# Kernel optimization log

Measured on AMD Instinct MI355X. Metric: run time of the kernel, lower is better.

Reference implementation:

```python
import jax, jax.numpy as jnp
import numpy as np
from jax import lax

B, C, K = 16, 320, 8  # batch, channels, template kernel size
EPS = 1e-12  # F.normalize eps


def _pool_to(x, k):
    # adaptive avg pool to (k, k); H, W are exact multiples of k here
    b, c, h, w = x.shape
    return x.reshape(b, c, k, h // k, k, w // k).mean(axis=(3, 5))


def _l2norm(x):
    # L2 normalize over channel dim (dim=1), matching F.normalize(p=2, dim=1)
    n = jnp.sqrt(jnp.sum(x * x, axis=1, keepdims=True))
    return x / jnp.maximum(n, EPS)


def _fusion(feats, w1, b1, w2, b2):
    # global avg pool -> 2-layer MLP score per template -> softmax -> weighted sum
    scores = jnp.concatenate(
        [jax.nn.relu(f.mean(axis=(2, 3)) @ w1 + b1) @ w2 + b2 for f in feats], axis=1
    )  # (B, 3)
    a = jax.nn.softmax(scores, axis=1)
    return sum(a[:, i, None, None, None] * feats[i] for i in range(3))


def _corr(template_kernel, search):
    # depthwise correlation + channel sum == per-sample VALID conv with a
    # single (1, C, K, K) kernel; vmap over batch
    tn = _l2norm(template_kernel)  # (B, C, K, K)
    sn = _l2norm(search)           # (B, C, H, W)

    def one(sb, tb):
        return lax.conv_general_dilated(
            sb[None], tb[None], (1, 1), 'VALID',
            dimension_numbers=('NCHW', 'OIHW', 'NCHW'))[0]  # (1, Ho, Wo)

    return jax.vmap(one)(sn, tn)  # (B, 1, Ho, Wo)


_SPECS = [
    ('t0_p3', (B, C, 32, 32)), ('t0_p4', (B, C, 16, 16)), ('t0_p5', (B, C, 8, 8)),
    ('t1_p3', (B, C, 32, 32)), ('t1_p4', (B, C, 16, 16)), ('t1_p5', (B, C, 8, 8)),
    ('t2_p3', (B, C, 32, 32)), ('t2_p4', (B, C, 16, 16)), ('t2_p5', (B, C, 8, 8)),
    ('s_p3', (B, C, 64, 64)), ('s_p4', (B, C, 32, 32)), ('s_p5', (B, C, 16, 16)),
]
_PARAMS = [
    ('fp3_w1', (C, C // 4)), ('fp3_b1', (C // 4,)), ('fp3_w2', (C // 4, 1)), ('fp3_b2', (1,)),
    ('fp4_w1', (C, C // 4)), ('fp4_b1', (C // 4,)), ('fp4_w2', (C // 4, 1)), ('fp4_b2', (1,)),
    ('fp5_w1', (C, C // 4)), ('fp5_b1', (C // 4,)), ('fp5_w2', (C // 4, 1)), ('fp5_b2', (1,)),
]


def setup_inputs() -> dict:
    key = jax.random.key(0)
    d = {}
    for i, (name, shape) in enumerate(_SPECS):
        d[name] = jax.random.normal(jax.random.fold_in(key, i), shape, jnp.float32)
    for j, (name, shape) in enumerate(_PARAMS):
        k = jax.random.fold_in(key, 100 + j)
        if name.endswith('b1') or name.endswith('b2'):
            d[name] = jnp.zeros(shape, jnp.float32)
        else:
            d[name] = jax.random.normal(k, shape, jnp.float32) * 0.05
    return d


def reference(t0_p3, t0_p4, t0_p5, t1_p3, t1_p4, t1_p5, t2_p3, t2_p4, t2_p5,
              s_p3, s_p4, s_p5,
              fp3_w1, fp3_b1, fp3_w2, fp3_b2,
              fp4_w1, fp4_b1, fp4_w2, fp4_b2,
              fp5_w1, fp5_b1, fp5_w2, fp5_b2):
    tp3 = _fusion([t0_p3, t1_p3, t2_p3], fp3_w1, fp3_b1, fp3_w2, fp3_b2)
    tp4 = _fusion([t0_p4, t1_p4, t2_p4], fp4_w1, fp4_b1, fp4_w2, fp4_b2)
    tp5 = _fusion([t0_p5, t1_p5, t2_p5], fp5_w1, fp5_b1, fp5_w2, fp5_b2)
    corr_p3 = _corr(_pool_to(tp3, K), s_p3)  # (B, 1, 57, 57)
    corr_p4 = _corr(_pool_to(tp4, K), s_p4)  # (B, 1, 25, 25)
    corr_p5 = _corr(_pool_to(tp5, K), s_p5)  # (B, 1, 9, 9)
    return (corr_p3, corr_p4, corr_p5)
```

## Files before the change

### kernel.cpp

```cpp
#include <hip/hip_runtime.h>
#include <math.h>

#define BATCH 16
#define CH 320

typedef __attribute__((ext_vector_type(8))) short bf16x8;
typedef __attribute__((ext_vector_type(4))) short shortx4;
typedef __attribute__((ext_vector_type(4))) float f32x4;

static constexpr size_t PLSZ     = (size_t)BATCH * CH * 64;
static constexpr size_t WS_POOL3 = 0;
static constexpr size_t WS_POOL4 = 3 * PLSZ;
static constexpr size_t WS_TF    = 6 * PLSZ;
static constexpr size_t WS_MEANS = 9 * PLSZ;
static constexpr size_t WS_AW    = WS_MEANS + 9 * BATCH * CH;
static constexpr size_t WS_PART  = WS_AW + 144;
static constexpr size_t WS_ABF   = WS_PART + 3 * BATCH * 80 * 64;
static constexpr size_t UB3 = 0;
static constexpr size_t UB4 = (size_t)BATCH * 64 * 4096;
static constexpr size_t UB5 = UB4 + (size_t)BATCH * 64 * 1024;

__device__ __forceinline__ float bf2f(unsigned short u) {
    union { unsigned int i; float f; } x; x.i = ((unsigned int)u) << 16; return x.f;
}
__device__ __forceinline__ unsigned short f2bf(float f) {
    union { float f; unsigned int i; } x; x.f = f;
    return (unsigned short)((x.i + 0x7FFFu + ((x.i >> 16) & 1u)) >> 16);
}

template <int HW, int KK>
__device__ __forceinline__ void pool_body(int idx, const float* __restrict__ a0,
                                          const float* __restrict__ a1, const float* __restrict__ a2,
                                          float* __restrict__ dst, float* __restrict__ means, int lane) {
    constexpr int NPL = BATCH * CH * 64;
    int tmpl = idx / NPL;
    int r = idx % NPL;
    const float* src = (tmpl == 0) ? a0 : ((tmpl == 1) ? a1 : a2);
    int bc = r >> 6;
    int pos = r & 63;
    int oh = pos >> 3, ow = pos & 7;
    const float* base = src + (size_t)bc * HW * HW;
    float s = 0.0f;
    if constexpr (KK == 4) {
#pragma unroll
        for (int i = 0; i < 4; ++i) {
            float4 v = *(const float4*)(base + (oh * 4 + i) * HW + ow * 4);
            s += v.x + v.y + v.z + v.w;
        }
    } else {
#pragma unroll
        for (int i = 0; i < 2; ++i) {
            float2 v = *(const float2*)(base + (oh * 2 + i) * HW + ow * 2);
            s += v.x + v.y;
        }
    }
    s *= (1.0f / (KK * KK));
    dst[idx] = s;
    float m = s;
#pragma unroll
    for (int o = 32; o; o >>= 1) m += __shfl_xor(m, o);
    if (lane == 0) means[tmpl * (BATCH * CH) + bc] = m * (1.0f / 64.0f);
}

__global__ __launch_bounds__(256) void prep_kernel(
    const float* __restrict__ t0p3, const float* __restrict__ t1p3, const float* __restrict__ t2p3,
    const float* __restrict__ t0p4, const float* __restrict__ t1p4, const float* __restrict__ t2p4,
    const float* __restrict__ t0p5, const float* __restrict__ t1p5, const float* __restrict__ t2p5,
    float* __restrict__ pool3, float* __restrict__ pool4, float* __restrict__ means) {
    int bid = blockIdx.x, t = threadIdx.x, lane = t & 63;
    if (bid < 3840) {
        pool_body<32, 4>(bid * 256 + t, t0p3, t1p3, t2p3, pool3, means, lane);
    } else if (bid < 7680) {
        pool_body<16, 2>((bid - 3840) * 256 + t, t0p4, t1p4, t2p4, pool4, means + 3 * BATCH * CH, lane);
    } else {
        int w = ((bid - 7680) * 256 + t) >> 6;
        constexpr int NR = BATCH * CH;
        int tmpl = w / NR, rem = w % NR;
        const float* src = (tmpl == 0) ? t0p5 : ((tmpl == 1) ? t1p5 : t2p5);
        float v = src[(size_t)rem * 64 + lane];
#pragma unroll
        for (int o = 32; o; o >>= 1) v += __shfl_xor(v, o);
        if (lane == 0) means[6 * BATCH * CH + w] = v * (1.0f / 64.0f);
    }
}

__global__ __launch_bounds__(256) void weights_kernel(const float* __restrict__ means,
        const float* w13, const float* b13, const float* w23, const float* b23,
        const float* w14, const float* b14, const float* w24, const float* b24,
        const float* w15, const float* b15, const float* w25, const float* b25,
        float* __restrict__ a_out) {
    __shared__ float m[3 * CH];
    __shared__ float hv[240];
    __shared__ float sc[3];
    int lvl = blockIdx.x / BATCH;
    int b = blockIdx.x % BATCH;
    int t = threadIdx.x;
    const float* w1 = (lvl == 0) ? w13 : ((lvl == 1) ? w14 : w15);
    const float* b1 = (lvl == 0) ? b13 : ((lvl == 1) ? b14 : b15);
    const float* w2 = (lvl == 0) ? w23 : ((lvl == 1) ? w24 : w25);
    const float* b2 = (lvl == 0) ? b23 : ((lvl == 1) ? b24 : b25);
    const float* mb = means + lvl * (3 * BATCH * CH);
    for (int j = t; j < 3 * CH; j += 256) {
        int i = j / CH, c = j % CH;
        m[j] = mb[i * (BATCH * CH) + b * CH + c];
    }
    __syncthreads();
    if (t < 240) {
        int i = t / 80, jj = t % 80;
        float acc = b1[jj];
#pragma unroll 4
        for (int c = 0; c < CH; ++c) acc = fmaf(m[i * CH + c], w1[c * 80 + jj], acc);
        hv[t] = fmaxf(acc, 0.0f) * w2[jj];
    }
    __syncthreads();
    if (t < 3) {
        float s = b2[0];
#pragma unroll 8
        for (int jj = 0; jj < 80; ++jj) s += hv[t * 80 + jj];
        sc[t] = s;
    }
    __syncthreads();
    if (t == 0) {
        float mx = fmaxf(sc[0], fmaxf(sc[1], sc[2]));
        float e0 = expf(sc[0] - mx), e1 = expf(sc[1] - mx), e2 = expf(sc[2] - mx);
        float inv = 1.0f / (e0 + e1 + e2);
        float* ao = a_out + lvl * 48 + b * 3;
        ao[0] = e0 * inv; ao[1] = e1 * inv; ao[2] = e2 * inv;
    }
}

__global__ __launch_bounds__(256) void fuse_kernel(
        const float* __restrict__ p30, const float* __restrict__ p31, const float* __restrict__ p32,
        const float* __restrict__ p40, const float* __restrict__ p41, const float* __restrict__ p42,
        const float* __restrict__ p50, const float* __restrict__ p51, const float* __restrict__ p52,
        const float* __restrict__ aw, float* __restrict__ tf, float* __restrict__ partial) {
    __shared__ float red[256];
    int lvl = blockIdx.x / 1280;
    int r = blockIdx.x % 1280;
    int t = threadIdx.x;
    const float* p0 = (lvl == 0) ? p30 : ((lvl == 1) ? p40 : p50);
    const float* p1 = (lvl == 0) ? p31 : ((lvl == 1) ? p41 : p51);
    const float* p2 = (lvl == 0) ? p32 : ((lvl == 1) ? p42 : p52);
    int idx = r * 256 + t;
    int b = r / 80;
    int j = r % 80;
    const float* ab = aw + lvl * 48 + b * 3;
    float a0 = ab[0], a1 = ab[1], a2 = ab[2];
    float v = a0 * p0[idx] + a1 * p1[idx] + a2 * p2[idx];
    tf[(size_t)lvl * PLSZ + idx] = v;
    red[t] = v * v;
    __syncthreads();
    if (t < 64) {
        float s = red[t] + red[t + 64] + red[t + 128] + red[t + 192];
        partial[((size_t)(lvl * BATCH + b) * 80 + j) * 64 + t] = s;
    }
}

__global__ __launch_bounds__(256) void atrans_kernel(const float* __restrict__ tf,
        const float* __restrict__ part, short* __restrict__ abf) {
    __shared__ float lds[64 * 68];
    __shared__ float red2[4 * 64];
    __shared__ float sv[64];
    int lvl = blockIdx.x >> 4;
    int b = blockIdx.x & 15;
    int t = threadIdx.x;
    {
        const float* p = part + ((size_t)(lvl * BATCH + b) * 80) * 64 + (t & 63);
        int jg = t >> 6;
        float s = 0.0f;
        for (int j = jg * 20; j < jg * 20 + 20; ++j) s += p[j * 64];
        red2[jg * 64 + (t & 63)] = s;
    }
    __syncthreads();
    if (t < 64) {
        float s = red2[t] + red2[64 + t] + red2[128 + t] + red2[192 + t];
        sv[t] = 1.0f / fmaxf(sqrtf(s), 1e-12f);
    }
    __syncthreads();
    const float* tb = tf + (size_t)lvl * PLSZ + (size_t)b * (CH * 64);
    short* ab = abf + ((size_t)(lvl * BATCH + b) * 64) * 320;
    for (int c0 = 0; c0 < 320; c0 += 64) {
        __syncthreads();
#pragma unroll
        for (int i = 0; i < 4; ++i) {
            int c = (t >> 4) + 16 * i;
            int p4 = (t & 15) * 4;
            *(float4*)(lds + c * 68 + p4) = *(const float4*)(tb + (size_t)(c0 + c) * 64 + p4);
        }
        __syncthreads();
        int p = t >> 2;
        int cs = (t & 3) * 16;
        float s_p = sv[p];
        bf16x8 o0, o1;
#pragma unroll
        for (int u = 0; u < 8; ++u) o0[u] = (short)f2bf(lds[(cs + u) * 68 + p] * s_p);
#pragma unroll
        for (int u = 0; u < 8; ++u) o1[u] = (short)f2bf(lds[(cs + 8 + u) * 68 + p] * s_p);
        *(bf16x8*)(ab + (size_t)p * 320 + c0 + cs) = o0;
        *(bf16x8*)(ab + (size_t)p * 320 + c0 + cs + 8) = o1;
    }
}

template <int H>
__device__ __forceinline__ void gemm_body(const float* __restrict__ S, const short* __restrict__ A,
                                          short* __restrict__ U, int bid,
                                          short* __restrict__ Bb, float* __restrict__ red,
                                          float* __restrict__ invs) {
    constexpr int N = H * H;
    constexpr int NBLK = N / 64;
    int b = bid / NBLK;
    int n0 = (bid % NBLK) * 64;
    int t = threadIdx.x;
    int w = t >> 6, l = t & 63, g = l >> 4, ln = l & 15;
    int cg = t >> 4;
    int nc = t & 15;
    const float* Sb = S + (size_t)b * CH * N + n0;
    const short* Ab = A + (size_t)b * 64 * 320;
    f32x4 acc[4];
#pragma unroll
    for (int i = 0; i < 4; ++i) acc[i] = (f32x4){0.f, 0.f, 0.f, 0.f};
    float ssq[4] = {0.f, 0.f, 0.f, 0.f};

    for (int kk = 0; kk < 320; kk += 32) {
        __syncthreads();
#pragma unroll
        for (int i = 0; i < 2; ++i) {
            int c = cg + 16 * i;
            float4 v = *(const float4*)(Sb + (size_t)(kk + c) * N + nc * 4);
            ssq[0] = fmaf(v.x, v.x, ssq[0]);
            ssq[1] = fmaf(v.y, v.y, ssq[1]);
            ssq[2] = fmaf(v.z, v.z, ssq[2]);
            ssq[3] = fmaf(v.w, v.w, ssq[3]);
            shortx4 h;
            h.x = (short)f2bf(v.x); h.y = (short)f2bf(v.y);
            h.z = (short)f2bf(v.z); h.w = (short)f2bf(v.w);
            *(shortx4*)(Bb + c * 76 + nc * 4) = h;
        }
        __syncthreads();
        bf16x8 af[4];
#pragma unroll
        for (int mt = 0; mt < 4; ++mt)
            af[mt] = *(const bf16x8*)(Ab + (mt * 16 + ln) * 320 + kk + 8 * g);
        bf16x8 bfr;
#pragma unroll
        for (int j = 0; j < 8; ++j) bfr[j] = Bb[(8 * g + j) * 76 + 16 * w + ln];
#pragma unroll
        for (int mt = 0; mt < 4; ++mt)
            acc[mt] = __builtin_amdgcn_mfma_f32_16x16x32_bf16(af[mt], bfr, acc[mt], 0, 0, 0);
    }
    red[cg * 64 + nc * 4 + 0] = ssq[0];
    red[cg * 64 + nc * 4 + 1] = ssq[1];
    red[cg * 64 + nc * 4 + 2] = ssq[2];
    red[cg * 64 + nc * 4 + 3] = ssq[3];
    __syncthreads();
    if (t < 64) {
        float s = 0.0f;
#pragma unroll
        for (int i = 0; i < 16; ++i) s += red[i * 64 + t];
        invs[t] = 1.0f / fmaxf(sqrtf(s), 1e-12f);
    }
    __syncthreads();
    float iv = invs[16 * w + ln];
#pragma unroll
    for (int mt = 0; mt < 4; ++mt) {
#pragma unroll
        for (int r = 0; r < 4; ++r) {
            int p = mt * 16 + 4 * g + r;
            U[(size_t)(b * 64 + p) * N + n0 + 16 * w + ln] = (short)f2bf(acc[mt][r] * iv);
        }
    }
}

__global__ __launch_bounds__(256) void gemm_kernel(const float* __restrict__ sp3,
        const float* __restrict__ sp4, const float* __restrict__ sp5,
        const short* __restrict__ abf, short* __restrict__ u) {
    __shared__ short Bb[32 * 76];
    __shared__ float red[16 * 64];
    __shared__ float invs[64];
    int bid = blockIdx.x;
    if (bid < 1024)      gemm_body<64>(sp3, abf,          u + UB3, bid,        Bb, red, invs);
    else if (bid < 1280) gemm_body<32>(sp4, abf + 327680, u + UB4, bid - 1024, Bb, red, invs);
    else                 gemm_body<16>(sp5, abf + 655360, u + UB5, bid - 1280, Bb, red, invs);
}

__global__ __launch_bounds__(256) void combine_kernel(const short* __restrict__ U,
                                                      float* __restrict__ out) {
    int tid = blockIdx.x * 256 + threadIdx.x;
    if (tid < 51984) {
        int b = tid / 3249, r = tid % 3249;
        int oh = r / 57, ow = r % 57;
        const short* u = U + UB3 + ((size_t)b * 64) * 4096 + oh * 64 + ow;
        float s = 0.0f;
#pragma unroll
        for (int kh = 0; kh < 8; ++kh)
#pragma unroll
            for (int kw = 0; kw < 8; ++kw)
                s += bf2f((unsigned short)u[(size_t)(kh * 8 + kw) * 4096 + kh * 64 + kw]);
        out[tid] = s;
    } else if (tid < 61984) {
        int x = tid - 51984;
        int b = x / 625, r = x % 625;
        int oh = r / 25, ow = r % 25;
        const short* u = U + UB4 + ((size_t)b * 64) * 1024 + oh * 32 + ow;
        float s = 0.0f;
#pragma unroll
        for (int kh = 0; kh < 8; ++kh)
#pragma unroll
            for (int kw = 0; kw < 8; ++kw)
                s += bf2f((unsigned short)u[(size_t)(kh * 8 + kw) * 1024 + kh * 32 + kw]);
        out[tid] = s;
    } else if (tid < 63280) {
        int x = tid - 61984;
        int b = x / 81, r = x % 81;
        int oh = r / 9, ow = r % 9;
        const short* u = U + UB5 + ((size_t)b * 64) * 256 + oh * 16 + ow;
        float s = 0.0f;
#pragma unroll
        for (int kh = 0; kh < 8; ++kh)
#pragma unroll
            for (int kw = 0; kw < 8; ++kw)
                s += bf2f((unsigned short)u[(size_t)(kh * 8 + kw) * 256 + kh * 16 + kw]);
        out[tid] = s;
    }
}

extern "C" void kernel_launch(void* const* d_in, const int* in_sizes, int n_in,
                              void* d_out, int out_size, void* d_ws, size_t ws_size,
                              hipStream_t stream) {
    const float* t0p3 = (const float*)d_in[0];
    const float* t0p4 = (const float*)d_in[1];
    const float* t0p5 = (const float*)d_in[2];
    const float* t1p3 = (const float*)d_in[3];
    const float* t1p4 = (const float*)d_in[4];
    const float* t1p5 = (const float*)d_in[5];
    const float* t2p3 = (const float*)d_in[6];
    const float* t2p4 = (const float*)d_in[7];
    const float* t2p5 = (const float*)d_in[8];
    const float* sp3  = (const float*)d_in[9];
    const float* sp4  = (const float*)d_in[10];
    const float* sp5  = (const float*)d_in[11];
    const float* f3w1 = (const float*)d_in[12];
    const float* f3b1 = (const float*)d_in[13];
    const float* f3w2 = (const float*)d_in[14];
    const float* f3b2 = (const float*)d_in[15];
    const float* f4w1 = (const float*)d_in[16];
    const float* f4b1 = (const float*)d_in[17];
    const float* f4w2 = (const float*)d_in[18];
    const float* f4b2 = (const float*)d_in[19];
    const float* f5w1 = (const float*)d_in[20];
    const float* f5b1 = (const float*)d_in[21];
    const float* f5w2 = (const float*)d_in[22];
    const float* f5b2 = (const float*)d_in[23];

    float* ws = (float*)d_ws;
    short* abf = (short*)(ws + WS_ABF);
    short* ubuf = (short*)ws;

    prep_kernel<<<11520, 256, 0, stream>>>(t0p3, t1p3, t2p3, t0p4, t1p4, t2p4,
                                           t0p5, t1p5, t2p5,
                                           ws + WS_POOL3, ws + WS_POOL4, ws + WS_MEANS);
    weights_kernel<<<48, 256, 0, stream>>>(ws + WS_MEANS,
                                           f3w1, f3b1, f3w2, f3b2,
                                           f4w1, f4b1, f4w2, f4b2,
                                           f5w1, f5b1, f5w2, f5b2, ws + WS_AW);
    fuse_kernel<<<3840, 256, 0, stream>>>(ws + WS_POOL3, ws + WS_POOL3 + PLSZ, ws + WS_POOL3 + 2 * PLSZ,
                                          ws + WS_POOL4, ws + WS_POOL4 + PLSZ, ws + WS_POOL4 + 2 * PLSZ,
                                          t0p5, t1p5, t2p5,
                                          ws + WS_AW, ws + WS_TF, ws + WS_PART);
    atrans_kernel<<<48, 256, 0, stream>>>(ws + WS_TF, ws + WS_PART, abf);
    gemm_kernel<<<1344, 256, 0, stream>>>(sp3, sp4, sp5, abf, ubuf);
    combine_kernel<<<248, 256, 0, stream>>>(ubuf, (float*)d_out);
}
```

Before: 97.06 us.

## Double-buffer search tile in LDS with transpose reads and position-major U layout

Rewrites the GEMM body so the search tile is double-buffered in LDS. The next k-slice's global loads and template fragment are prefetched while the current MFMAs run, leaving one barrier per step instead of two. It swaps operand roles so search positions form the M dimension, reads them with ds_read_b64_tr_b16 transpose loads, and packs bf16 with v_cvt_pk_bf16_f32. The intermediate U buffer becomes position-major (64 template taps contiguous per position), and the combine kernel's indexing is updated to match. In exchange it relies on inline asm, manual waitcnt and sched barriers, and a changed store pattern for U.

```diff
diff --git a/kernel.cpp b/kernel.cpp
--- a/kernel.cpp
+++ b/kernel.cpp
@@ -5,8 +5,9 @@
 #define CH 320
 
 typedef __attribute__((ext_vector_type(8))) short bf16x8;
-typedef __attribute__((ext_vector_type(4))) short shortx4;
 typedef __attribute__((ext_vector_type(4))) float f32x4;
+
+union FragU { bf16x8 f; unsigned long long u[2]; };
 
 static constexpr size_t PLSZ     = (size_t)BATCH * CH * 64;
 static constexpr size_t WS_POOL3 = 0;
@@ -17,8 +18,8 @@
 static constexpr size_t WS_PART  = WS_AW + 144;
 static constexpr size_t WS_ABF   = WS_PART + 3 * BATCH * 80 * 64;
 static constexpr size_t UB3 = 0;
-static constexpr size_t UB4 = (size_t)BATCH * 64 * 4096;
-static constexpr size_t UB5 = UB4 + (size_t)BATCH * 64 * 1024;
+static constexpr size_t UB4 = (size_t)BATCH * 4096 * 64;
+static constexpr size_t UB5 = UB4 + (size_t)BATCH * 1024 * 64;
 
 __device__ __forceinline__ float bf2f(unsigned short u) {
     union { unsigned int i; float f; } x; x.i = ((unsigned int)u) << 16; return x.f;
@@ -26,6 +27,11 @@
 __device__ __forceinline__ unsigned short f2bf(float f) {
     union { float f; unsigned int i; } x; x.f = f;
     return (unsigned short)((x.i + 0x7FFFu + ((x.i >> 16) & 1u)) >> 16);
+}
+__device__ __forceinline__ unsigned cvtpk(float lo, float hi) {
+    unsigned r;
+    asm("v_cvt_pk_bf16_f32 %0, %1, %2" : "=v"(r) : "v"(lo), "v"(hi));
+    return r;
 }
 
 template <int HW, int KK>
@@ -202,56 +208,86 @@
 }
 
 template <int H>
-__device__ __forceinline__ void gemm_body(const float* __restrict__ S, const short* __restrict__ A,
-                                          short* __restrict__ U, int bid,
-                                          short* __restrict__ Bb, float* __restrict__ red,
-                                          float* __restrict__ invs) {
+__device__ __forceinline__ void gemm_body(const float* __restrict__ S, const short* __restrict__ T,
+                                          short* __restrict__ V, int bid,
+                                          unsigned short* St, float* red, float* invs) {
     constexpr int N = H * H;
-    constexpr int NBLK = N / 64;
-    int b = bid / NBLK;
-    int n0 = (bid % NBLK) * 64;
+    constexpr int XB = N / 64;
+    int b = bid / XB;
+    int x0b = (bid % XB) * 64;
     int t = threadIdx.x;
     int w = t >> 6, l = t & 63, g = l >> 4, ln = l & 15;
     int cg = t >> 4;
-    int nc = t & 15;
-    const float* Sb = S + (size_t)b * CH * N + n0;
-    const short* Ab = A + (size_t)b * 64 * 320;
+    int x0 = (t & 15) * 4;
+
+    const float* Sb = S + (size_t)b * CH * N + x0b;
+    const short* Tp = T + ((size_t)b * 64 + 16 * w + ln) * 320 + 8 * g;
+
     f32x4 acc[4];
 #pragma unroll
     for (int i = 0; i < 4; ++i) acc[i] = (f32x4){0.f, 0.f, 0.f, 0.f};
     float ssq[4] = {0.f, 0.f, 0.f, 0.f};
 
-    for (int kk = 0; kk < 320; kk += 32) {
-        __syncthreads();
-#pragma unroll
-        for (int i = 0; i < 2; ++i) {
-            int c = cg + 16 * i;
-            float4 v = *(const float4*)(Sb + (size_t)(kk + c) * N + nc * 4);
-            ssq[0] = fmaf(v.x, v.x, ssq[0]);
-            ssq[1] = fmaf(v.y, v.y, ssq[1]);
-            ssq[2] = fmaf(v.z, v.z, ssq[2]);
-            ssq[3] = fmaf(v.w, v.w, ssq[3]);
-            shortx4 h;
-            h.x = (short)f2bf(v.x); h.y = (short)f2bf(v.y);
-            h.z = (short)f2bf(v.z); h.w = (short)f2bf(v.w);
-            *(shortx4*)(Bb + c * 76 + nc * 4) = h;
-        }
-        __syncthreads();
-        bf16x8 af[4];
-#pragma unroll
-        for (int mt = 0; mt < 4; ++mt)
-            af[mt] = *(const bf16x8*)(Ab + (mt * 16 + ln) * 320 + kk + 8 * g);
-        bf16x8 bfr;
-#pragma unroll
-        for (int j = 0; j < 8; ++j) bfr[j] = Bb[(8 * g + j) * 76 + 16 * w + ln];
-#pragma unroll
-        for (int mt = 0; mt < 4; ++mt)
-            acc[mt] = __builtin_amdgcn_mfma_f32_16x16x32_bf16(af[mt], bfr, acc[mt], 0, 0, 0);
-    }
-    red[cg * 64 + nc * 4 + 0] = ssq[0];
-    red[cg * 64 + nc * 4 + 1] = ssq[1];
-    red[cg * 64 + nc * 4 + 2] = ssq[2];
-    red[cg * 64 + nc * 4 + 3] = ssq[3];
+    unsigned trbase = (unsigned)(size_t)St + (unsigned)(g * 256 + ln * 8);
+    int e1 = ((x0 >> 4) * 8 + (cg >> 2)) * 64 + (cg & 3) * 16 + (x0 & 15);
+
+    {
+        const float* p = Sb + (size_t)cg * N + x0;
+        float4 v1 = *(const float4*)(p);
+        float4 v2 = *(const float4*)(p + (size_t)16 * N);
+        ssq[0] = fmaf(v1.x, v1.x, fmaf(v2.x, v2.x, ssq[0]));
+        ssq[1] = fmaf(v1.y, v1.y, fmaf(v2.y, v2.y, ssq[1]));
+        ssq[2] = fmaf(v1.z, v1.z, fmaf(v2.z, v2.z, ssq[2]));
+        ssq[3] = fmaf(v1.w, v1.w, fmaf(v2.w, v2.w, ssq[3]));
+        *(uint2*)(St + e1)       = (uint2){cvtpk(v1.x, v1.y), cvtpk(v1.z, v1.w)};
+        *(uint2*)(St + e1 + 256) = (uint2){cvtpk(v2.x, v2.y), cvtpk(v2.z, v2.w)};
+    }
+    bf16x8 tcur = *(const bf16x8*)(Tp);
+    __syncthreads();
+
+#define TRRD2(FR, OFF) \
+    asm volatile("ds_read_b64_tr_b16 %0, %2 offset:%c3\n\tds_read_b64_tr_b16 %1, %2 offset:%c4" \
+                 : "=v"((FR).u[0]), "=v"((FR).u[1]) : "v"(trbase), "i"(OFF), "i"((OFF) + 128));
+
+#define GSTEP(BUF, S_) { \
+    int kn = 32 * ((S_) + 1); \
+    bool dost = kn < 320; \
+    int kl = dost ? kn : 288; \
+    const float* p_ = Sb + (size_t)(kl + cg) * N + x0; \
+    float4 v1 = *(const float4*)(p_); \
+    float4 v2 = *(const float4*)(p_ + (size_t)16 * N); \
+    bf16x8 tnx = *(const bf16x8*)(Tp + kl); \
+    FragU fr0, fr1, fr2, fr3; \
+    TRRD2(fr0, (BUF) * 4096 + 0) \
+    TRRD2(fr1, (BUF) * 4096 + 1024) \
+    TRRD2(fr2, (BUF) * 4096 + 2048) \
+    TRRD2(fr3, (BUF) * 4096 + 3072) \
+    asm volatile("s_waitcnt lgkmcnt(0)" ::: "memory"); \
+    __builtin_amdgcn_sched_barrier(0); \
+    acc[0] = __builtin_amdgcn_mfma_f32_16x16x32_bf16(fr0.f, tcur, acc[0], 0, 0, 0); \
+    acc[1] = __builtin_amdgcn_mfma_f32_16x16x32_bf16(fr1.f, tcur, acc[1], 0, 0, 0); \
+    acc[2] = __builtin_amdgcn_mfma_f32_16x16x32_bf16(fr2.f, tcur, acc[2], 0, 0, 0); \
+    acc[3] = __builtin_amdgcn_mfma_f32_16x16x32_bf16(fr3.f, tcur, acc[3], 0, 0, 0); \
+    if (dost) { \
+        ssq[0] = fmaf(v1.x, v1.x, fmaf(v2.x, v2.x, ssq[0])); \
+        ssq[1] = fmaf(v1.y, v1.y, fmaf(v2.y, v2.y, ssq[1])); \
+        ssq[2] = fmaf(v1.z, v1.z, fmaf(v2.z, v2.z, ssq[2])); \
+        ssq[3] = fmaf(v1.w, v1.w, fmaf(v2.w, v2.w, ssq[3])); \
+        unsigned short* d_ = St + (((BUF) ^ 1) * 2048) + e1; \
+        *(uint2*)(d_)       = (uint2){cvtpk(v1.x, v1.y), cvtpk(v1.z, v1.w)}; \
+        *(uint2*)(d_ + 256) = (uint2){cvtpk(v2.x, v2.y), cvtpk(v2.z, v2.w)}; \
+    } \
+    tcur = tnx; \
+    __syncthreads(); }
+
+    for (int s = 0; s < 10; s += 2) {
+        GSTEP(0, s)
+        GSTEP(1, s + 1)
+    }
+#undef GSTEP
+#undef TRRD2
+
+    *(f32x4*)(red + cg * 64 + x0) = (f32x4){ssq[0], ssq[1], ssq[2], ssq[3]};
     __syncthreads();
     if (t < 64) {
         float s = 0.0f;
@@ -260,27 +296,27 @@
         invs[t] = 1.0f / fmaxf(sqrtf(s), 1e-12f);
     }
     __syncthreads();
-    float iv = invs[16 * w + ln];
+
+    short* Vb = V + ((size_t)b * N + x0b) * 64 + 16 * w + ln;
 #pragma unroll
     for (int mt = 0; mt < 4; ++mt) {
-#pragma unroll
-        for (int r = 0; r < 4; ++r) {
-            int p = mt * 16 + 4 * g + r;
-            U[(size_t)(b * 64 + p) * N + n0 + 16 * w + ln] = (short)f2bf(acc[mt][r] * iv);
-        }
+        f32x4 iv = *(f32x4*)(invs + mt * 16 + 4 * g);
+#pragma unroll
+        for (int r = 0; r < 4; ++r)
+            Vb[(size_t)(mt * 16 + 4 * g + r) * 64] = (short)f2bf(acc[mt][r] * iv[r]);
     }
 }
 
 __global__ __launch_bounds__(256) void gemm_kernel(const float* __restrict__ sp3,
         const float* __restrict__ sp4, const float* __restrict__ sp5,
         const short* __restrict__ abf, short* __restrict__ u) {
-    __shared__ short Bb[32 * 76];
+    __shared__ unsigned short St[2 * 2048];
     __shared__ float red[16 * 64];
     __shared__ float invs[64];
     int bid = blockIdx.x;
-    if (bid < 1024)      gemm_body<64>(sp3, abf,          u + UB3, bid,        Bb, red, invs);
-    else if (bid < 1280) gemm_body<32>(sp4, abf + 327680, u + UB4, bid - 1024, Bb, red, invs);
-    else                 gemm_body<16>(sp5, abf + 655360, u + UB5, bid - 1280, Bb, red, invs);
+    if (bid < 1024)      gemm_body<64>(sp3, abf,          u + UB3, bid,        St, red, invs);
+    else if (bid < 1280) gemm_body<32>(sp4, abf + 327680, u + UB4, bid - 1024, St, red, invs);
+    else                 gemm_body<16>(sp5, abf + 655360, u + UB5, bid - 1280, St, red, invs);
 }
 
 __global__ __launch_bounds__(256) void combine_kernel(const short* __restrict__ U,
@@ -289,37 +325,37 @@
     if (tid < 51984) {
         int b = tid / 3249, r = tid % 3249;
         int oh = r / 57, ow = r % 57;
-        const short* u = U + UB3 + ((size_t)b * 64) * 4096 + oh * 64 + ow;
+        const short* u = U + UB3 + ((size_t)b * 4096 + oh * 64 + ow) * 64;
         float s = 0.0f;
 #pragma unroll
         for (int kh = 0; kh < 8; ++kh)
 #pragma unroll
             for (int kw = 0; kw < 8; ++kw)
-                s += bf2f((unsigned short)u[(size_t)(kh * 8 + kw) * 4096 + kh * 64 + kw]);
+                s += bf2f((unsigned short)u[(kh * 64 + kw) * 64 + kh * 8 + kw]);
         out[tid] = s;
     } else if (tid < 61984) {
         int x = tid - 51984;
         int b = x / 625, r = x % 625;
         int oh = r / 25, ow = r % 25;
-        const short* u = U + UB4 + ((size_t)b * 64) * 1024 + oh * 32 + ow;
+        const short* u = U + UB4 + ((size_t)b * 1024 + oh * 32 + ow) * 64;
         float s = 0.0f;
 #pragma unroll
         for (int kh = 0; kh < 8; ++kh)
 #pragma unroll
             for (int kw = 0; kw < 8; ++kw)
-                s += bf2f((unsigned short)u[(size_t)(kh * 8 + kw) * 1024 + kh * 32 + kw]);
+                s += bf2f((unsigned short)u[(kh * 32 + kw) * 64 + kh * 8 + kw]);
         out[tid] = s;
     } else if (tid < 63280) {
         int x = tid - 61984;
         int b = x / 81, r = x % 81;
         int oh = r / 9, ow = r % 9;
-        const short* u = U + UB5 + ((size_t)b * 64) * 256 + oh * 16 + ow;
+        const short* u = U + UB5 + ((size_t)b * 256 + oh * 16 + ow) * 64;
         float s = 0.0f;
 #pragma unroll
         for (int kh = 0; kh < 8; ++kh)
 #pragma unroll
             for (int kw = 0; kw < 8; ++kw)
-                s += bf2f((unsigned short)u[(size_t)(kh * 8 + kw) * 256 + kh * 16 + kw]);
+                s += bf2f((unsigned short)u[(kh * 16 + kw) * 64 + kh * 8 + kw]);
         out[tid] = s;
     }
 }
```

After: 89.38 us. 1.09x faster.
